# Kernel optimization log

Hardware: AMD Instinct MI355X
Metric: run time of the kernel (lower is better)

Reference implementation:

```python
import jax, jax.numpy as jnp
import numpy as np

BATCH = 2048
DIM = 1024       # discrete_dim
EMBED = 512
HID = 2 * EMBED  # MLP hidden width per source: [embed_dim*2, embed_dim*2, discrete_dim]
NUM_STEPS = 32


def setup_inputs() -> dict:
    key = jax.random.key(0)
    ks = jax.random.split(key, 8)
    s = 0.02  # init scale for weights
    init_samples = jax.random.randint(ks[0], (BATCH, DIM), 0, 2).astype(jnp.float32)
    target_pos = jax.random.randint(ks[1], (NUM_STEPS, BATCH), 0, DIM, dtype=jnp.int32)
    W1 = jax.random.normal(ks[2], (DIM, HID), jnp.float32) * s
    b1 = jnp.zeros((HID,), jnp.float32)
    W2 = jax.random.normal(ks[3], (HID, HID), jnp.float32) * s
    b2 = jnp.zeros((HID,), jnp.float32)
    W3 = jax.random.normal(ks[4], (HID, DIM), jnp.float32) * s
    b3 = jnp.zeros((DIM,), jnp.float32)
    return {
        "init_samples": init_samples, "target_pos": target_pos,
        "W1": W1, "b1": b1, "W2": W2, "b2": b2, "W3": W3, "b3": b3,
        "num_steps": NUM_STEPS,
    }


def _mlp(x, W1, b1, W2, b2, W3, b3):
    h = jax.nn.relu(x @ W1 + b1)
    h = jax.nn.relu(h @ W2 + b2)
    return h @ W3 + b3  # pos logits, [B, DIM]


def reference(init_samples, target_pos, W1, b1, W2, b2, W3, b3, num_steps):
    B = init_samples.shape[0]
    rows = jnp.arange(B)
    very_init_samples = init_samples
    total_log0 = jnp.zeros((B, 1), init_samples.dtype)  # mode != 'forward': total_log = 0.0

    def step(carry, tpos):
        samples, total_log = carry
        log_pos_prob = jax.nn.log_softmax(_mlp(samples, W1, b1, W2, b2, W3, b3), axis=-1)
        log_target = jnp.take_along_axis(log_pos_prob, tpos[:, None], axis=1)  # [B,1]
        total_log = total_log + log_target
        orig_bit = samples[rows, tpos]                       # gather, [B]
        samples = samples.at[rows, tpos].set(1.0 - orig_bit)  # scatter bit flip
        return (samples, total_log), tpos

    (final_samples, total_log), delta = jax.lax.scan(
        step, (init_samples, total_log0), target_pos[:num_steps])
    return final_samples, delta, total_log, very_init_samples
```

## Files before the change

kernel.cpp:

```cpp
#include <hip/hip_runtime.h>
#include <stdint.h>

#define BATCH 2048
#define NDIM  1024
#define HID   1024
#define TSTEPS 32

#define OUT_FINAL 0
#define OUT_DELTA 2097152
#define OUT_TOTAL 2162688
#define OUT_VINIT 2164736

#define SC_ROWSUM 0
#define SC_TGT    8192
#define SC_TOTAL  16384
#define SC_BIAS   24576
#define SC_FLAG   36864

#define WF_WT1    0u
#define WF_WT2    2097152u
#define WF_WT3    4194304u
#define WF_A1     6291456u
#define WF_BIAS   14680064u
#define WF_SIGNS  14692352u
#define WF_ROWSUM 14757888u
#define WF_TGT    15020032u
#define WF_FLAG   15282176u
#define WF_H1     15286272u

__device__ __forceinline__ float bf2f(ushort u) {
  union { uint32_t u; float f; } v; v.u = ((uint32_t)u) << 16; return v.f;
}
__device__ __forceinline__ ushort f2bf(float f) {
  union { float f; uint32_t u; } v; v.f = f;
  uint32_t u = v.u;
  u += 0x7fffu + ((u >> 16) & 1u);
  return (ushort)(u >> 16);
}

typedef __attribute__((ext_vector_type(8))) short bf16x8;
typedef __attribute__((ext_vector_type(8))) unsigned short u16x8;
typedef __attribute__((ext_vector_type(4))) float f32x4;

__global__ __launch_bounds__(256) void flag_k(const void* __restrict__ init,
                                              uint32_t* __restrict__ flag) {
  const ushort* p = (const ushort*)init;
  __shared__ uint32_t acc[256];
  uint32_t a = 0;
  for (int i = threadIdx.x; i < 32768; i += 256) a |= p[2 * i];
  acc[threadIdx.x] = a;
  __syncthreads();
  for (int s = 128; s > 0; s >>= 1) {
    if (threadIdx.x < s) acc[threadIdx.x] |= acc[threadIdx.x + s];
    __syncthreads();
  }
  if (threadIdx.x == 0) *flag = (acc[0] != 0) ? 1u : 0u;
}

__global__ __launch_bounds__(256) void zero_k(float* __restrict__ p) {
  p[blockIdx.x * 256 + threadIdx.x] = 0.f;
}

__global__ __launch_bounds__(256) void canon_b_k(const void* b1, const void* b2,
                                                 const void* b3,
                                                 float* __restrict__ dst,
                                                 const uint32_t* __restrict__ flag) {
  const void* src = (blockIdx.x == 0) ? b1 : (blockIdx.x == 1) ? b2 : b3;
  float* d = dst + blockIdx.x * 1024;
  const bool isbf = (*flag != 0);
  for (int i = threadIdx.x; i < 1024; i += 256)
    d[i] = isbf ? bf2f(((const ushort*)src)[i]) : ((const float*)src)[i];
}

__global__ __launch_bounds__(256) void canon_w3_k(const void* __restrict__ S1,
                                                  const void* __restrict__ S2,
                                                  const void* __restrict__ S3,
                                                  ushort* __restrict__ D,
                                                  const uint32_t* __restrict__ flag) {
  __shared__ ushort tile[32][33];
  const void* S = (blockIdx.z == 0) ? S1 : (blockIdx.z == 1) ? S2 : S3;
  ushort* Dz = D + (size_t)blockIdx.z * 1024 * 1024;
  const int bx = blockIdx.x * 32, by = blockIdx.y * 32;
  const int tx = threadIdx.x, ty = threadIdx.y;
  const bool isbf = (*flag != 0);
  #pragma unroll
  for (int i = 0; i < 32; i += 8) {
    const size_t idx = (size_t)(by + ty + i) * 1024 + bx + tx;
    tile[ty + i][tx] = isbf ? ((const ushort*)S)[idx] : f2bf(((const float*)S)[idx]);
  }
  __syncthreads();
  #pragma unroll
  for (int i = 0; i < 32; i += 8)
    Dz[(size_t)(bx + ty + i) * 1024 + by + tx] = tile[tx][ty + i];
}

__global__ __launch_bounds__(256) void sign_k(const void* __restrict__ init,
                                              const int* __restrict__ tpos,
                                              uint8_t* __restrict__ signs,
                                              float* __restrict__ rowsum,
                                              float* __restrict__ tgt,
                                              const uint32_t* __restrict__ flag) {
  const int m = blockIdx.x, tid = threadIdx.x;
  const bool isbf = (*flag != 0);
  __shared__ float bits[NDIM];
  #pragma unroll
  for (int i = 0; i < 4; ++i) {
    const int k = tid + i * 256;
    bits[k] = isbf ? bf2f(((const ushort*)init)[(size_t)m * NDIM + k])
                   : ((const float*)init)[(size_t)m * NDIM + k];
  }
  __syncthreads();
  if (tid == 0) {
    for (int t = 0; t < TSTEPS; ++t) {
      const int tp = tpos[t * BATCH + m];
      const float b = bits[tp];
      signs[t * BATCH + m] = (uint8_t)(b != 0.f);
      bits[tp] = 1.f - b;
    }
  }
  if (tid < 32) rowsum[m * 32 + tid] = 0.f;
  else if (tid < 64) tgt[m * 32 + (tid - 32)] = 0.f;
}

template <int ASTAGE, int EPI>
__global__ __launch_bounds__(256) void gemm_bt(const void* __restrict__ A,
                                               const ushort* __restrict__ Bt,
                                               const float* __restrict__ bias,
                                               void* __restrict__ Cout,
                                               const int* __restrict__ tpos,
                                               float* __restrict__ rowsum,
                                               float* __restrict__ tgt,
                                               const uint32_t* __restrict__ flag,
                                               int rowbase) {
  constexpr int BM = 128, BN = 128, BK = 32, LS = 40, K = 1024;
  __shared__ ushort Asm[BM * LS];
  __shared__ ushort Bsm[BN * LS];
  const int tid = threadIdx.x;
  const int wave = tid >> 6, lane = tid & 63;
  const int q = lane >> 4, r = lane & 15;

  const int lid = blockIdx.y * gridDim.x + blockIdx.x;
  const int xcd = lid & 7;
  const int sl  = lid >> 3;
  const int mb  = xcd + 8 * (sl >> 3);
  const int nb  = sl & 7;
  const int n0 = nb * BN;
  const int m0 = mb * BM;
  const int wm = (wave & 1) * 64, wn = (wave >> 1) * 64;

  f32x4 acc[4][4];
  #pragma unroll
  for (int i = 0; i < 4; ++i)
    #pragma unroll
    for (int j = 0; j < 4; ++j)
      #pragma unroll
      for (int e = 0; e < 4; ++e) acc[i][j][e] = 0.f;

  const int row = tid >> 2, c8 = (tid & 3) * 8;
  const bool isbf = (ASTAGE == 1) ? (*flag != 0) : true;

  u16x8 pa0, pa1, pb0, pb1;
  {
    if constexpr (ASTAGE == 1) {
      if (isbf) {
        pa0 = *(const u16x8*)((const ushort*)A + (size_t)(m0 + row) * K + c8);
        pa1 = *(const u16x8*)((const ushort*)A + (size_t)(m0 + 64 + row) * K + c8);
      } else {
        const float* p0 = (const float*)A + (size_t)(m0 + row) * K + c8;
        const float* p1 = (const float*)A + (size_t)(m0 + 64 + row) * K + c8;
        const float4 fa = *(const float4*)p0, fb = *(const float4*)(p0 + 4);
        const float4 fc = *(const float4*)p1, fd = *(const float4*)(p1 + 4);
        pa0[0] = f2bf(fa.x); pa0[1] = f2bf(fa.y); pa0[2] = f2bf(fa.z); pa0[3] = f2bf(fa.w);
        pa0[4] = f2bf(fb.x); pa0[5] = f2bf(fb.y); pa0[6] = f2bf(fb.z); pa0[7] = f2bf(fb.w);
        pa1[0] = f2bf(fc.x); pa1[1] = f2bf(fc.y); pa1[2] = f2bf(fc.z); pa1[3] = f2bf(fc.w);
        pa1[4] = f2bf(fd.x); pa1[5] = f2bf(fd.y); pa1[6] = f2bf(fd.z); pa1[7] = f2bf(fd.w);
      }
    } else {
      pa0 = *(const u16x8*)((const ushort*)A + (size_t)(m0 + row) * K + c8);
      pa1 = *(const u16x8*)((const ushort*)A + (size_t)(m0 + 64 + row) * K + c8);
    }
    pb0 = *(const u16x8*)(Bt + (size_t)(n0 + row) * K + c8);
    pb1 = *(const u16x8*)(Bt + (size_t)(n0 + 64 + row) * K + c8);
  }

  for (int k0 = 0; k0 < K; k0 += BK) {
    __syncthreads();
    *(u16x8*)(Asm + row * LS + c8) = pa0;
    *(u16x8*)(Asm + (64 + row) * LS + c8) = pa1;
    *(u16x8*)(Bsm + row * LS + c8) = pb0;
    *(u16x8*)(Bsm + (64 + row) * LS + c8) = pb1;
    {
      const int kn = (k0 + BK) & (K - 1);
      if constexpr (ASTAGE == 1) {
        if (isbf) {
          pa0 = *(const u16x8*)((const ushort*)A + (size_t)(m0 + row) * K + kn + c8);
          pa1 = *(const u16x8*)((const ushort*)A + (size_t)(m0 + 64 + row) * K + kn + c8);
        } else {
          const float* p0 = (const float*)A + (size_t)(m0 + row) * K + kn + c8;
          const float* p1 = (const float*)A + (size_t)(m0 + 64 + row) * K + kn + c8;
          const float4 fa = *(const float4*)p0, fb = *(const float4*)(p0 + 4);
          const float4 fc = *(const float4*)p1, fd = *(const float4*)(p1 + 4);
          pa0[0] = f2bf(fa.x); pa0[1] = f2bf(fa.y); pa0[2] = f2bf(fa.z); pa0[3] = f2bf(fa.w);
          pa0[4] = f2bf(fb.x); pa0[5] = f2bf(fb.y); pa0[6] = f2bf(fb.z); pa0[7] = f2bf(fb.w);
          pa1[0] = f2bf(fc.x); pa1[1] = f2bf(fc.y); pa1[2] = f2bf(fc.z); pa1[3] = f2bf(fc.w);
          pa1[4] = f2bf(fd.x); pa1[5] = f2bf(fd.y); pa1[6] = f2bf(fd.z); pa1[7] = f2bf(fd.w);
        }
      } else {
        pa0 = *(const u16x8*)((const ushort*)A + (size_t)(m0 + row) * K + kn + c8);
        pa1 = *(const u16x8*)((const ushort*)A + (size_t)(m0 + 64 + row) * K + kn + c8);
      }
      pb0 = *(const u16x8*)(Bt + (size_t)(n0 + row) * K + kn + c8);
      pb1 = *(const u16x8*)(Bt + (size_t)(n0 + 64 + row) * K + kn + c8);
    }
    __syncthreads();
    bf16x8 af[4], bfr[4];
    #pragma unroll
    for (int t = 0; t < 4; ++t) {
      af[t]  = *(const bf16x8*)(Asm + (wm + t * 16 + r) * LS + q * 8);
      bfr[t] = *(const bf16x8*)(Bsm + (wn + t * 16 + r) * LS + q * 8);
    }
    #pragma unroll
    for (int mt = 0; mt < 4; ++mt)
      #pragma unroll
      for (int nt = 0; nt < 4; ++nt)
        acc[mt][nt] = __builtin_amdgcn_mfma_f32_16x16x32_bf16(af[mt], bfr[nt], acc[mt][nt], 0, 0, 0);
  }

  #pragma unroll
  for (int mt = 0; mt < 4; ++mt) {
    #pragma unroll
    for (int reg = 0; reg < 4; ++reg) {
      const int grow = m0 + wm + mt * 16 + q * 4 + reg;
      if constexpr (EPI == 2) {
        const int growg = rowbase + grow;
        const int tp = tpos[growg];
        float s2 = 0.f;
        #pragma unroll
        for (int nt = 0; nt < 4; ++nt) {
          const int gcol = n0 + wn + nt * 16 + r;
          const float v = acc[mt][nt][reg] + bias[gcol];
          if (gcol == tp) tgt[growg] = v;
          s2 += __expf(v);
        }
        s2 += __shfl_xor(s2, 1);
        s2 += __shfl_xor(s2, 2);
        s2 += __shfl_xor(s2, 4);
        s2 += __shfl_xor(s2, 8);
        if (r == 0) atomicAdd(&rowsum[growg], s2);
      } else {
        #pragma unroll
        for (int nt = 0; nt < 4; ++nt) {
          const int gcol = n0 + wn + nt * 16 + r;
          const float v = acc[mt][nt][reg] + bias[gcol];
          if constexpr (EPI == 0) {
            ((float*)Cout)[(size_t)grow * NDIM + gcol] = v;
          } else {
            ((ushort*)Cout)[(size_t)grow * NDIM + gcol] = f2bf(v > 0.f ? v : 0.f);
          }
        }
      }
    }
  }
}

__global__ __launch_bounds__(256) void build_h1(float* __restrict__ a1,
                                                const void* __restrict__ W1,
                                                const uint8_t* __restrict__ signs,
                                                const int* __restrict__ tpos,
                                                ushort* __restrict__ h1,
                                                const uint32_t* __restrict__ flag,
                                                int t0, int nsteps) {
  const int m = blockIdx.x;
  const int k = threadIdx.x * 4;
  const bool isbf = (*flag != 0);
  float4 a = *(const float4*)(a1 + (size_t)m * HID + k);
  for (int t = 0; t < nsteps; ++t) {
    ushort4 h;
    h.x = f2bf(a.x > 0.f ? a.x : 0.f);
    h.y = f2bf(a.y > 0.f ? a.y : 0.f);
    h.z = f2bf(a.z > 0.f ? a.z : 0.f);
    h.w = f2bf(a.w > 0.f ? a.w : 0.f);
    *(ushort4*)(h1 + ((size_t)(t * BATCH + m)) * HID + k) = h;
    const int tg = t0 + t;
    const int tp = tpos[tg * BATCH + m];
    const float s = 1.f - 2.f * (float)signs[tg * BATCH + m];
    float wx, wy, wz, ww;
    if (isbf) {
      const ushort4 wv = *(const ushort4*)((const ushort*)W1 + (size_t)tp * HID + k);
      wx = bf2f(wv.x); wy = bf2f(wv.y); wz = bf2f(wv.z); ww = bf2f(wv.w);
    } else {
      const float4 wv = *(const float4*)((const float*)W1 + (size_t)tp * HID + k);
      wx = wv.x; wy = wv.y; wz = wv.z; ww = wv.w;
    }
    a.x += s * wx; a.y += s * wy; a.z += s * wz; a.w += s * ww;
  }
  *(float4*)(a1 + (size_t)m * HID + k) = a;
}

__global__ __launch_bounds__(256) void outputs_k(const void* __restrict__ init,
                                                 const int* __restrict__ tpos,
                                                 const float* __restrict__ tgt,
                                                 const float* __restrict__ rowsum,
                                                 float* __restrict__ out,
                                                 const uint32_t* __restrict__ flag) {
  const int m = blockIdx.x;
  const int tid = threadIdx.x;
  const int k = tid * 4;
  const bool isbf = (*flag != 0);
  float v[4];
  if (isbf) {
    const ushort4 iv = *(const ushort4*)((const ushort*)init + (size_t)m * NDIM + k);
    v[0] = bf2f(iv.x); v[1] = bf2f(iv.y); v[2] = bf2f(iv.z); v[3] = bf2f(iv.w);
  } else {
    const float4 iv = *(const float4*)((const float*)init + (size_t)m * NDIM + k);
    v[0] = iv.x; v[1] = iv.y; v[2] = iv.z; v[3] = iv.w;
  }
  float4 o0; o0.x = v[0]; o0.y = v[1]; o0.z = v[2]; o0.w = v[3];
  *(float4*)(out + OUT_VINIT + (size_t)m * NDIM + k) = o0;
  for (int t = 0; t < TSTEPS; ++t) {
    const int tp = tpos[t * BATCH + m];
    if ((tp >> 2) == tid) v[tp & 3] = 1.f - v[tp & 3];
  }
  float4 o; o.x = v[0]; o.y = v[1]; o.z = v[2]; o.w = v[3];
  *(float4*)(out + OUT_FINAL + (size_t)m * NDIM + k) = o;
  if (tid < 32) out[OUT_DELTA + m * 32 + tid] = (float)tpos[m * 32 + tid];
  if (tid < 64) {
    const int t = tid & 31;
    float s = tgt[t * BATCH + m] - logf(rowsum[t * BATCH + m]);
    s += __shfl_xor(s, 1, 32);
    s += __shfl_xor(s, 2, 32);
    s += __shfl_xor(s, 4, 32);
    s += __shfl_xor(s, 8, 32);
    s += __shfl_xor(s, 16, 32);
    if (tid == 0) out[OUT_TOTAL + m] = s;
  }
}

template <int ASRC, int EPI>
__global__ __launch_bounds__(256) void gemm_t(const void* __restrict__ A,
                                              const void* __restrict__ W,
                                              const float* __restrict__ bias,
                                              ushort* __restrict__ Cout,
                                              const int* __restrict__ tpos,
                                              float* __restrict__ rowsum,
                                              float* __restrict__ tgt,
                                              const uint32_t* __restrict__ flag,
                                              int tstep) {
  constexpr int BM = 64, BN = 64, BK = 32, BKP = 40, K = 1024;
  __shared__ ushort Asm[BM * BKP];
  __shared__ ushort Bsm[BN * BKP];
  const int tid = threadIdx.x;
  const int w = tid >> 6, lane = tid & 63;
  const int q = lane >> 4, r = lane & 15;
  const int n0 = blockIdx.x * BN;
  const int m0 = blockIdx.y * BM;
  const bool isbf = (*flag != 0);
  const int srow = tid >> 2, scol = (tid & 3) * 8;
  const int kk = tid >> 3, ng = (tid & 7) * 8;

  f32x4 acc[4];
  #pragma unroll
  for (int nt = 0; nt < 4; ++nt)
    #pragma unroll
    for (int e = 0; e < 4; ++e) acc[nt][e] = 0.f;

  for (int k0 = 0; k0 < K; k0 += BK) {
    u16x8 av;
    if constexpr (ASRC == 0) {
      if (isbf) {
        av = *(const u16x8*)((const ushort*)A + (size_t)(m0 + srow) * K + k0 + scol);
      } else {
        const float* fp = (const float*)A + (size_t)(m0 + srow) * K + k0 + scol;
        const float4 fa = *(const float4*)fp, fb = *(const float4*)(fp + 4);
        av[0] = f2bf(fa.x); av[1] = f2bf(fa.y); av[2] = f2bf(fa.z); av[3] = f2bf(fa.w);
        av[4] = f2bf(fb.x); av[5] = f2bf(fb.y); av[6] = f2bf(fb.z); av[7] = f2bf(fb.w);
      }
    } else {
      av = *(const u16x8*)((const ushort*)A + (size_t)(m0 + srow) * K + k0 + scol);
      if constexpr (ASRC == 1) {
        #pragma unroll
        for (int e = 0; e < 8; ++e) av[e] = (av[e] & 0x8000u) ? (unsigned short)0 : av[e];
      }
    }
    ushort bw[8];
    if (isbf) {
      const u16x8 wv = *(const u16x8*)((const ushort*)W + (size_t)(k0 + kk) * NDIM + n0 + ng);
      #pragma unroll
      for (int j = 0; j < 8; ++j) bw[j] = wv[j];
    } else {
      const float* fp = (const float*)W + (size_t)(k0 + kk) * NDIM + n0 + ng;
      const float4 fa = *(const float4*)fp, fb = *(const float4*)(fp + 4);
      bw[0] = f2bf(fa.x); bw[1] = f2bf(fa.y); bw[2] = f2bf(fa.z); bw[3] = f2bf(fa.w);
      bw[4] = f2bf(fb.x); bw[5] = f2bf(fb.y); bw[6] = f2bf(fb.z); bw[7] = f2bf(fb.w);
    }
    __syncthreads();
    *(u16x8*)(Asm + srow * BKP + scol) = av;
    #pragma unroll
    for (int j = 0; j < 8; ++j) Bsm[(ng + j) * BKP + kk] = bw[j];
    __syncthreads();
    const bf16x8 af = *(const bf16x8*)(Asm + (w * 16 + r) * BKP + q * 8);
    #pragma unroll
    for (int nt = 0; nt < 4; ++nt) {
      const bf16x8 bfr = *(const bf16x8*)(Bsm + (nt * 16 + r) * BKP + q * 8);
      acc[nt] = __builtin_amdgcn_mfma_f32_16x16x32_bf16(af, bfr, acc[nt], 0, 0, 0);
    }
  }

  if constexpr (EPI == 2) {
    #pragma unroll
    for (int reg = 0; reg < 4; ++reg) {
      const int grow = m0 + w * 16 + q * 4 + reg;
      const int tp = tpos[tstep * BATCH + grow];
      float s = 0.f;
      #pragma unroll
      for (int nt = 0; nt < 4; ++nt) {
        const int gcol = n0 + nt * 16 + r;
        const float v = acc[nt][reg] + bias[gcol];
        if (gcol == tp) tgt[grow] = v;
        s += __expf(v);
      }
      s += __shfl_xor(s, 1);
      s += __shfl_xor(s, 2);
      s += __shfl_xor(s, 4);
      s += __shfl_xor(s, 8);
      if (r == 0) atomicAdd(&rowsum[grow], s);
    }
  } else {
    #pragma unroll
    for (int nt = 0; nt < 4; ++nt) {
      #pragma unroll
      for (int reg = 0; reg < 4; ++reg) {
        const int grow = m0 + w * 16 + q * 4 + reg;
        const int gcol = n0 + nt * 16 + r;
        float v = acc[nt][reg] + bias[gcol];
        if constexpr (EPI == 1) v = (v > 0.f) ? v : 0.f;
        Cout[(size_t)grow * NDIM + gcol] = f2bf(v);
      }
    }
  }
}

__global__ __launch_bounds__(256) void step_k(ushort* __restrict__ a1,
                                              const void* __restrict__ init,
                                              const void* __restrict__ W1,
                                              const int* __restrict__ tpos,
                                              float* __restrict__ rowsum,
                                              const float* __restrict__ tgt,
                                              float* __restrict__ total,
                                              const uint32_t* __restrict__ flag,
                                              int t) {
  const int m = blockIdx.x;
  const int k = threadIdx.x * 4;
  const bool isbf = (*flag != 0);
  const int tp = tpos[t * BATCH + m];
  const float b0 = isbf ? bf2f(((const ushort*)init)[(size_t)m * NDIM + tp])
                        : ((const float*)init)[(size_t)m * NDIM + tp];
  int cnt = 0;
  for (int u = 0; u < t; ++u) cnt += (tpos[u * BATCH + m] == tp) ? 1 : 0;
  const float bit = (cnt & 1) ? (1.f - b0) : b0;
  const float s = 1.f - 2.f * bit;
  float wx, wy, wz, ww;
  if (isbf) {
    const ushort4 wv = *(const ushort4*)((const ushort*)W1 + (size_t)tp * HID + k);
    wx = bf2f(wv.x); wy = bf2f(wv.y); wz = bf2f(wv.z); ww = bf2f(wv.w);
  } else {
    const float4 wv = *(const float4*)((const float*)W1 + (size_t)tp * HID + k);
    wx = wv.x; wy = wv.y; wz = wv.z; ww = wv.w;
  }
  ushort4 a = *(const ushort4*)(a1 + (size_t)m * HID + k);
  a.x = f2bf(bf2f(a.x) + s * wx);
  a.y = f2bf(bf2f(a.y) + s * wy);
  a.z = f2bf(bf2f(a.z) + s * wz);
  a.w = f2bf(bf2f(a.w) + s * ww);
  *(ushort4*)(a1 + (size_t)m * HID + k) = a;
  if (threadIdx.x == 0) {
    total[m] += tgt[m] - logf(rowsum[m]);
    rowsum[m] = 0.f;
  }
}

__global__ __launch_bounds__(256) void finalize_k(const float* __restrict__ total,
                                                  float* __restrict__ out_total) {
  const int m = blockIdx.x * 256 + threadIdx.x;
  out_total[m] = total[m];
}

__global__ __launch_bounds__(256) void out_final_k(const void* __restrict__ init,
                                                   const int* __restrict__ tpos,
                                                   float* __restrict__ out,
                                                   const uint32_t* __restrict__ flag) {
  const int m = blockIdx.x;
  const int k = threadIdx.x * 4;
  const bool isbf = (*flag != 0);
  float v[4];
  if (isbf) {
    const ushort4 iv = *(const ushort4*)((const ushort*)init + (size_t)m * NDIM + k);
    v[0] = bf2f(iv.x); v[1] = bf2f(iv.y); v[2] = bf2f(iv.z); v[3] = bf2f(iv.w);
  } else {
    const float4 iv = *(const float4*)((const float*)init + (size_t)m * NDIM + k);
    v[0] = iv.x; v[1] = iv.y; v[2] = iv.z; v[3] = iv.w;
  }
  for (int t = 0; t < TSTEPS; ++t) {
    const int tp = tpos[t * BATCH + m];
    if ((tp >> 2) == (int)threadIdx.x) v[tp & 3] = 1.f - v[tp & 3];
  }
  float4 o; o.x = v[0]; o.y = v[1]; o.z = v[2]; o.w = v[3];
  *(float4*)(out + OUT_FINAL + (size_t)m * NDIM + k) = o;
}

__global__ __launch_bounds__(256) void out_vinit_k(const void* __restrict__ init,
                                                   float* __restrict__ out,
                                                   const uint32_t* __restrict__ flag) {
  const int i = (blockIdx.x * 256 + threadIdx.x) * 4;
  float4 o;
  if (*flag) {
    const ushort4 iv = *(const ushort4*)((const ushort*)init + i);
    o.x = bf2f(iv.x); o.y = bf2f(iv.y); o.z = bf2f(iv.z); o.w = bf2f(iv.w);
  } else {
    o = *(const float4*)((const float*)init + i);
  }
  *(float4*)(out + OUT_VINIT + i) = o;
}

__global__ __launch_bounds__(256) void out_delta_k(const int* __restrict__ tpos,
                                                   float* __restrict__ out) {
  const int i = blockIdx.x * 256 + threadIdx.x;
  out[OUT_DELTA + i] = (float)tpos[i];
}

extern "C" void kernel_launch(void* const* d_in, const int* in_sizes, int n_in,
                              void* d_out, int out_size, void* d_ws, size_t ws_size,
                              hipStream_t stream) {
  const void* init = d_in[0];
  const int* tpos  = (const int*)d_in[1];
  const void* W1 = d_in[2];
  const void* b1 = d_in[3];
  const void* W2 = d_in[4];
  const void* b2 = d_in[5];
  const void* W3 = d_in[6];
  const void* b3 = d_in[7];
  float* out = (float*)d_out;
  char* ws = (char*)d_ws;

  const size_t MB = 1024ull * 1024ull;
  int CH = TSTEPS;
  while (CH > 1 && (size_t)WF_H1 + (size_t)CH * 8 * MB > ws_size) CH >>= 1;
  const bool fast = (ws_size >= (size_t)WF_H1 + 8 * MB);

  if (fast) {
    ushort*   WT1    = (ushort*)(ws + WF_WT1);
    ushort*   WT2    = (ushort*)(ws + WF_WT2);
    ushort*   WT3    = (ushort*)(ws + WF_WT3);
    float*    a1f    = (float*)(ws + WF_A1);
    float*    biases = (float*)(ws + WF_BIAS);
    uint8_t*  signs  = (uint8_t*)(ws + WF_SIGNS);
    float*    rowsum = (float*)(ws + WF_ROWSUM);
    float*    tgt    = (float*)(ws + WF_TGT);
    uint32_t* flag   = (uint32_t*)(ws + WF_FLAG);
    ushort*   h1     = (ushort*)(ws + WF_H1);
    ushort*   h2     = (ushort*)(ws + WF_H1 + (size_t)CH * 4 * MB);

    flag_k<<<1, 256, 0, stream>>>(init, flag);
    canon_b_k<<<3, 256, 0, stream>>>(b1, b2, b3, biases, flag);
    canon_w3_k<<<dim3(32, 32, 3), dim3(32, 8), 0, stream>>>(W1, W2, W3, WT1, flag);
    sign_k<<<BATCH, 256, 0, stream>>>(init, tpos, signs, rowsum, tgt, flag);

    gemm_bt<1, 0><<<dim3(8, 16), 256, 0, stream>>>(init, WT1, biases + 0, a1f,
                                                   nullptr, nullptr, nullptr, flag, 0);

    for (int t0 = 0; t0 < TSTEPS; t0 += CH) {
      build_h1<<<BATCH, 256, 0, stream>>>(a1f, W1, signs, tpos, h1, flag, t0, CH);
      gemm_bt<0, 1><<<dim3(8, CH * 16), 256, 0, stream>>>(h1, WT2, biases + 1024, h2,
                                                          nullptr, nullptr, nullptr, flag, 0);
      gemm_bt<0, 2><<<dim3(8, CH * 16), 256, 0, stream>>>(h2, WT3, biases + 2048, nullptr,
                                                          tpos, rowsum, tgt, flag, t0 * BATCH);
    }
    outputs_k<<<BATCH, 256, 0, stream>>>(init, tpos, tgt, rowsum, out, flag);
  } else {
    ushort*   a1     = (ushort*)(out + OUT_FINAL);
    ushort*   h2     = (ushort*)(out + OUT_VINIT);
    char*     sc     = (char*)(out + OUT_DELTA);
    float*    rowsum = (float*)(sc + SC_ROWSUM);
    float*    tgt    = (float*)(sc + SC_TGT);
    float*    total  = (float*)(sc + SC_TOTAL);
    float*    biases = (float*)(sc + SC_BIAS);
    uint32_t* flag   = (uint32_t*)(sc + SC_FLAG);

    flag_k<<<1, 256, 0, stream>>>(init, flag);
    zero_k<<<24, 256, 0, stream>>>(rowsum);
    canon_b_k<<<3, 256, 0, stream>>>(b1, b2, b3, biases, flag);
    gemm_t<0, 0><<<dim3(16, 32), 256, 0, stream>>>(init, W1, biases + 0, a1,
                                                   nullptr, nullptr, nullptr, flag, 0);
    for (int t = 0; t < TSTEPS; ++t) {
      gemm_t<1, 1><<<dim3(16, 32), 256, 0, stream>>>(a1, W2, biases + 1024, h2,
                                                     nullptr, nullptr, nullptr, flag, 0);
      gemm_t<2, 2><<<dim3(16, 32), 256, 0, stream>>>(h2, W3, biases + 2048, nullptr,
                                                     tpos, rowsum, tgt, flag, t);
      step_k<<<BATCH, 256, 0, stream>>>(a1, init, W1, tpos, rowsum, tgt, total, flag, t);
    }
    finalize_k<<<8, 256, 0, stream>>>(total, out + OUT_TOTAL);
    out_final_k<<<BATCH, 256, 0, stream>>>(init, tpos, out, flag);
    out_vinit_k<<<2048, 256, 0, stream>>>(init, out, flag);
    out_delta_k<<<256, 256, 0, stream>>>(tpos, out);
  }
}
```

Baseline: 592.0 us.

## Use direct global-to-LDS loads and 512-thread blocks in bt GEMM

Rewrites the main bf16 GEMM to stage A and B tiles with global_load_lds (direct global-to-LDS DMA) instead of register prefetch plus an LDS store. The block grows to 512 threads in 8 waves, each computing a 64x32 sub-tile, so each wave holds half as many accumulators. The padded LDS stride is dropped and the register double-buffer prefetch is removed, so loads are no longer overlapped with the MFMA work. The unpadded layout risks LDS bank conflicts, and the loop now syncs twice per k-step with no prefetch.

New measurement: 573.5 us. 3.1% less time.

```diff
diff --git a/kernel.cpp b/kernel.cpp
--- a/kernel.cpp
+++ b/kernel.cpp
@@ -41,6 +41,11 @@
 typedef __attribute__((ext_vector_type(8))) short bf16x8;
 typedef __attribute__((ext_vector_type(8))) unsigned short u16x8;
 typedef __attribute__((ext_vector_type(4))) float f32x4;
+
+__device__ __forceinline__ void gload_lds16(const void* g, void* l) {
+  __builtin_amdgcn_global_load_lds((const __attribute__((address_space(1))) void*)g,
+                                   (__attribute__((address_space(3))) void*)l, 16, 0, 0);
+}
 
 __global__ __launch_bounds__(256) void flag_k(const void* __restrict__ init,
                                               uint32_t* __restrict__ flag) {
@@ -123,7 +128,7 @@
 }
 
 template <int ASTAGE, int EPI>
-__global__ __launch_bounds__(256) void gemm_bt(const void* __restrict__ A,
+__global__ __launch_bounds__(512) void gemm_bt(const void* __restrict__ A,
                                                const ushort* __restrict__ Bt,
                                                const float* __restrict__ bias,
                                                void* __restrict__ Cout,
@@ -132,11 +137,11 @@
                                                float* __restrict__ tgt,
                                                const uint32_t* __restrict__ flag,
                                                int rowbase) {
-  constexpr int BM = 128, BN = 128, BK = 32, LS = 40, K = 1024;
-  __shared__ ushort Asm[BM * LS];
-  __shared__ ushort Bsm[BN * LS];
+  constexpr int BM = 128, BN = 128, BK = 32, K = 1024;
+  __shared__ ushort Asm[BM * BK];
+  __shared__ ushort Bsm[BN * BK];
   const int tid = threadIdx.x;
-  const int wave = tid >> 6, lane = tid & 63;
+  const int w = tid >> 6, lane = tid & 63;
   const int q = lane >> 4, r = lane & 15;
 
   const int lid = blockIdx.y * gridDim.x + blockIdx.x;
@@ -146,84 +151,52 @@
   const int nb  = sl & 7;
   const int n0 = nb * BN;
   const int m0 = mb * BM;
-  const int wm = (wave & 1) * 64, wn = (wave >> 1) * 64;
-
-  f32x4 acc[4][4];
+  const int wm = (w & 1) * 64;
+  const int wn = (w >> 1) * 32;
+
+  f32x4 acc[4][2];
   #pragma unroll
   for (int i = 0; i < 4; ++i)
     #pragma unroll
-    for (int j = 0; j < 4; ++j)
+    for (int j = 0; j < 2; ++j)
       #pragma unroll
       for (int e = 0; e < 4; ++e) acc[i][j][e] = 0.f;
 
   const int row = tid >> 2, c8 = (tid & 3) * 8;
   const bool isbf = (ASTAGE == 1) ? (*flag != 0) : true;
 
-  u16x8 pa0, pa1, pb0, pb1;
-  {
-    if constexpr (ASTAGE == 1) {
+  for (int k0 = 0; k0 < K; k0 += BK) {
+    if constexpr (ASTAGE == 0) {
+      gload_lds16((const char*)A + ((size_t)(m0 + row) * K + k0 + c8) * 2,
+                  (char*)Asm + tid * 16);
+    } else {
+      u16x8 av;
       if (isbf) {
-        pa0 = *(const u16x8*)((const ushort*)A + (size_t)(m0 + row) * K + c8);
-        pa1 = *(const u16x8*)((const ushort*)A + (size_t)(m0 + 64 + row) * K + c8);
+        av = *(const u16x8*)((const ushort*)A + (size_t)(m0 + row) * K + k0 + c8);
       } else {
-        const float* p0 = (const float*)A + (size_t)(m0 + row) * K + c8;
-        const float* p1 = (const float*)A + (size_t)(m0 + 64 + row) * K + c8;
-        const float4 fa = *(const float4*)p0, fb = *(const float4*)(p0 + 4);
-        const float4 fc = *(const float4*)p1, fd = *(const float4*)(p1 + 4);
-        pa0[0] = f2bf(fa.x); pa0[1] = f2bf(fa.y); pa0[2] = f2bf(fa.z); pa0[3] = f2bf(fa.w);
-        pa0[4] = f2bf(fb.x); pa0[5] = f2bf(fb.y); pa0[6] = f2bf(fb.z); pa0[7] = f2bf(fb.w);
-        pa1[0] = f2bf(fc.x); pa1[1] = f2bf(fc.y); pa1[2] = f2bf(fc.z); pa1[3] = f2bf(fc.w);
-        pa1[4] = f2bf(fd.x); pa1[5] = f2bf(fd.y); pa1[6] = f2bf(fd.z); pa1[7] = f2bf(fd.w);
+        const float* fp = (const float*)A + (size_t)(m0 + row) * K + k0 + c8;
+        const float4 fa = *(const float4*)fp, fb = *(const float4*)(fp + 4);
+        av[0] = f2bf(fa.x); av[1] = f2bf(fa.y); av[2] = f2bf(fa.z); av[3] = f2bf(fa.w);
+        av[4] = f2bf(fb.x); av[5] = f2bf(fb.y); av[6] = f2bf(fb.z); av[7] = f2bf(fb.w);
       }
-    } else {
-      pa0 = *(const u16x8*)((const ushort*)A + (size_t)(m0 + row) * K + c8);
-      pa1 = *(const u16x8*)((const ushort*)A + (size_t)(m0 + 64 + row) * K + c8);
-    }
-    pb0 = *(const u16x8*)(Bt + (size_t)(n0 + row) * K + c8);
-    pb1 = *(const u16x8*)(Bt + (size_t)(n0 + 64 + row) * K + c8);
-  }
-
-  for (int k0 = 0; k0 < K; k0 += BK) {
+      *(u16x8*)((char*)Asm + tid * 16) = av;
+    }
+    gload_lds16((const char*)Bt + ((size_t)(n0 + row) * K + k0 + c8) * 2,
+                (char*)Bsm + tid * 16);
     __syncthreads();
-    *(u16x8*)(Asm + row * LS + c8) = pa0;
-    *(u16x8*)(Asm + (64 + row) * LS + c8) = pa1;
-    *(u16x8*)(Bsm + row * LS + c8) = pb0;
-    *(u16x8*)(Bsm + (64 + row) * LS + c8) = pb1;
-    {
-      const int kn = (k0 + BK) & (K - 1);
-      if constexpr (ASTAGE == 1) {
-        if (isbf) {
-          pa0 = *(const u16x8*)((const ushort*)A + (size_t)(m0 + row) * K + kn + c8);
-          pa1 = *(const u16x8*)((const ushort*)A + (size_t)(m0 + 64 + row) * K + kn + c8);
-        } else {
-          const float* p0 = (const float*)A + (size_t)(m0 + row) * K + kn + c8;
-          const float* p1 = (const float*)A + (size_t)(m0 + 64 + row) * K + kn + c8;
-          const float4 fa = *(const float4*)p0, fb = *(const float4*)(p0 + 4);
-          const float4 fc = *(const float4*)p1, fd = *(const float4*)(p1 + 4);
-          pa0[0] = f2bf(fa.x); pa0[1] = f2bf(fa.y); pa0[2] = f2bf(fa.z); pa0[3] = f2bf(fa.w);
-          pa0[4] = f2bf(fb.x); pa0[5] = f2bf(fb.y); pa0[6] = f2bf(fb.z); pa0[7] = f2bf(fb.w);
-          pa1[0] = f2bf(fc.x); pa1[1] = f2bf(fc.y); pa1[2] = f2bf(fc.z); pa1[3] = f2bf(fc.w);
-          pa1[4] = f2bf(fd.x); pa1[5] = f2bf(fd.y); pa1[6] = f2bf(fd.z); pa1[7] = f2bf(fd.w);
-        }
-      } else {
-        pa0 = *(const u16x8*)((const ushort*)A + (size_t)(m0 + row) * K + kn + c8);
-        pa1 = *(const u16x8*)((const ushort*)A + (size_t)(m0 + 64 + row) * K + kn + c8);
-      }
-      pb0 = *(const u16x8*)(Bt + (size_t)(n0 + row) * K + kn + c8);
-      pb1 = *(const u16x8*)(Bt + (size_t)(n0 + 64 + row) * K + kn + c8);
-    }
-    __syncthreads();
-    bf16x8 af[4], bfr[4];
-    #pragma unroll
-    for (int t = 0; t < 4; ++t) {
-      af[t]  = *(const bf16x8*)(Asm + (wm + t * 16 + r) * LS + q * 8);
-      bfr[t] = *(const bf16x8*)(Bsm + (wn + t * 16 + r) * LS + q * 8);
-    }
+    bf16x8 af[4], bfr[2];
+    #pragma unroll
+    for (int t = 0; t < 4; ++t)
+      af[t] = *(const bf16x8*)(Asm + (wm + t * 16 + r) * BK + q * 8);
+    #pragma unroll
+    for (int t = 0; t < 2; ++t)
+      bfr[t] = *(const bf16x8*)(Bsm + (wn + t * 16 + r) * BK + q * 8);
     #pragma unroll
     for (int mt = 0; mt < 4; ++mt)
       #pragma unroll
-      for (int nt = 0; nt < 4; ++nt)
+      for (int nt = 0; nt < 2; ++nt)
         acc[mt][nt] = __builtin_amdgcn_mfma_f32_16x16x32_bf16(af[mt], bfr[nt], acc[mt][nt], 0, 0, 0);
+    __syncthreads();
   }
 
   #pragma unroll
@@ -236,7 +209,7 @@
         const int tp = tpos[growg];
         float s2 = 0.f;
         #pragma unroll
-        for (int nt = 0; nt < 4; ++nt) {
+        for (int nt = 0; nt < 2; ++nt) {
           const int gcol = n0 + wn + nt * 16 + r;
           const float v = acc[mt][nt][reg] + bias[gcol];
           if (gcol == tp) tgt[growg] = v;
@@ -249,7 +222,7 @@
         if (r == 0) atomicAdd(&rowsum[growg], s2);
       } else {
         #pragma unroll
-        for (int nt = 0; nt < 4; ++nt) {
+        for (int nt = 0; nt < 2; ++nt) {
           const int gcol = n0 + wn + nt * 16 + r;
           const float v = acc[mt][nt][reg] + bias[gcol];
           if constexpr (EPI == 0) {
@@ -565,14 +538,14 @@
     canon_w3_k<<<dim3(32, 32, 3), dim3(32, 8), 0, stream>>>(W1, W2, W3, WT1, flag);
     sign_k<<<BATCH, 256, 0, stream>>>(init, tpos, signs, rowsum, tgt, flag);
 
-    gemm_bt<1, 0><<<dim3(8, 16), 256, 0, stream>>>(init, WT1, biases + 0, a1f,
+    gemm_bt<1, 0><<<dim3(8, 16), 512, 0, stream>>>(init, WT1, biases + 0, a1f,
                                                    nullptr, nullptr, nullptr, flag, 0);
 
     for (int t0 = 0; t0 < TSTEPS; t0 += CH) {
       build_h1<<<BATCH, 256, 0, stream>>>(a1f, W1, signs, tpos, h1, flag, t0, CH);
-      gemm_bt<0, 1><<<dim3(8, CH * 16), 256, 0, stream>>>(h1, WT2, biases + 1024, h2,
+      gemm_bt<0, 1><<<dim3(8, CH * 16), 512, 0, stream>>>(h1, WT2, biases + 1024, h2,
                                                           nullptr, nullptr, nullptr, flag, 0);
-      gemm_bt<0, 2><<<dim3(8, CH * 16), 256, 0, stream>>>(h2, WT3, biases + 2048, nullptr,
+      gemm_bt<0, 2><<<dim3(8, CH * 16), 512, 0, stream>>>(h2, WT3, biases + 2048, nullptr,
                                                           tpos, rowsum, tgt, flag, t0 * BATCH);
     }
     outputs_k<<<BATCH, 256, 0, stream>>>(init, tpos, tgt, rowsum, out, flag);
```
